# Kernel tuning notes

Hardware: AMD Instinct MI355X
Metric: run time of the kernel (lower is better)

Reference implementation:

```python
import jax, jax.numpy as jnp
import numpy as np

D = 1024
NH = 16
HD = D // NH
DFF = 4 * D
EPS = 1e-5


def setup_inputs() -> dict:
    key = jax.random.key(0)
    ks = jax.random.split(key, 12)
    s = lambda fan_in: 1.0 / np.sqrt(fan_in)
    return {
        "x": jax.random.normal(ks[0], (2, 2048, D), dtype=jnp.float32),
        # weights stored [in, out] (transpose of torch Linear layout)
        "w_qkv": jax.random.uniform(ks[1], (D, 3 * D), minval=-s(D), maxval=s(D)),
        "w_proj": jax.random.uniform(ks[2], (D, D), minval=-s(D), maxval=s(D)),
        "ln1_w": jnp.ones((D,), jnp.float32),
        "ln1_b": jnp.zeros((D,), jnp.float32),
        "ln2_w": jnp.ones((D,), jnp.float32),
        "ln2_b": jnp.zeros((D,), jnp.float32),
        "fc1_w": jax.random.uniform(ks[3], (D, DFF), minval=-s(D), maxval=s(D)),
        "fc1_b": jax.random.uniform(ks[4], (DFF,), minval=-s(D), maxval=s(D)),
        "fc2_w": jax.random.uniform(ks[5], (DFF, D), minval=-s(DFF), maxval=s(DFF)),
        "fc2_b": jax.random.uniform(ks[6], (D,), minval=-s(DFF), maxval=s(DFF)),
    }


def _layernorm(x, w, b):
    mu = jnp.mean(x, axis=-1, keepdims=True)
    var = jnp.mean(jnp.square(x - mu), axis=-1, keepdims=True)
    return (x - mu) * jax.lax.rsqrt(var + EPS) * w + b


def _attn(x, w_qkv, w_proj):
    B, T, C = x.shape
    qkv = x @ w_qkv  # [B,T,3C]
    q, k, v = jnp.split(qkv, 3, axis=-1)
    q = q.reshape(B, T, NH, HD).transpose(0, 2, 1, 3)  # [B,nh,T,hd]
    k = k.reshape(B, T, NH, HD).transpose(0, 2, 1, 3)
    v = v.reshape(B, T, NH, HD).transpose(0, 2, 1, 3)
    att = jnp.einsum("bhqd,bhkd->bhqk", q, k) / np.sqrt(HD)
    causal = jnp.tril(jnp.ones((T, T), bool))
    att = jnp.where(causal, att, -jnp.inf)
    att = jax.nn.softmax(att, axis=-1)
    out = jnp.einsum("bhqk,bhkd->bhqd", att, v)
    out = out.transpose(0, 2, 1, 3).reshape(B, T, C)
    return out @ w_proj


def reference(x, w_qkv, w_proj, ln1_w, ln1_b, ln2_w, ln2_b, fc1_w, fc1_b, fc2_w, fc2_b):
    x = x + _attn(_layernorm(x, ln1_w, ln1_b), w_qkv, w_proj)
    h = _layernorm(x, ln2_w, ln2_b)
    h = jax.nn.gelu(h @ fc1_w + fc1_b, approximate=False) @ fc2_w + fc2_b
    return x + h
```

## Files before the change

kernel.cpp:

```cpp
#include <hip/hip_runtime.h>


typedef short  bf16x8 __attribute__((ext_vector_type(8)));
typedef short  bf16x4 __attribute__((ext_vector_type(4)));
typedef float  fx4    __attribute__((ext_vector_type(4)));
typedef int    ix2    __attribute__((ext_vector_type(2)));

#define DEV static __device__ __forceinline__

DEV short f2bf(float f) {
    unsigned u = __builtin_bit_cast(unsigned, f);
    u += 0x7fffu + ((u >> 16) & 1u);
    return (short)(u >> 16);
}

#define AS1(p) ((__attribute__((address_space(1))) void*)(p))
#define AS3(p) ((__attribute__((address_space(3))) void*)(p))

__global__ __launch_bounds__(256) void ln_kernel(const float* __restrict__ x,
                                                 const float* __restrict__ w,
                                                 const float* __restrict__ b,
                                                 short* __restrict__ out)
{
    int row = blockIdx.x;
    int tid = threadIdx.x;
    const float4 v = *(const float4*)(x + (size_t)row * 1024 + tid * 4);
    float s = v.x + v.y + v.z + v.w;
    float q = v.x * v.x + v.y * v.y + v.z * v.z + v.w * v.w;
#pragma unroll
    for (int off = 32; off > 0; off >>= 1) {
        s += __shfl_down(s, off);
        q += __shfl_down(q, off);
    }
    __shared__ float ls[4], lq[4];
    if ((tid & 63) == 0) { ls[tid >> 6] = s; lq[tid >> 6] = q; }
    __syncthreads();
    float S  = ls[0] + ls[1] + ls[2] + ls[3];
    float Q  = lq[0] + lq[1] + lq[2] + lq[3];
    float mu  = S * (1.0f / 1024.0f);
    float var = Q * (1.0f / 1024.0f) - mu * mu;
    float inv = rsqrtf(var + 1e-5f);
    float4 wv = *(const float4*)(w + tid * 4);
    float4 bv = *(const float4*)(b + tid * 4);
    bf16x4 o;
    o[0] = f2bf((v.x - mu) * inv * wv.x + bv.x);
    o[1] = f2bf((v.y - mu) * inv * wv.y + bv.y);
    o[2] = f2bf((v.z - mu) * inv * wv.z + bv.z);
    o[3] = f2bf((v.w - mu) * inv * wv.w + bv.w);
    *(bf16x4*)(out + (size_t)row * 1024 + tid * 4) = o;
}

__global__ __launch_bounds__(256) void transpose_f32_bf16(const float* __restrict__ in,
                                                          short* __restrict__ out,
                                                          int R, int C)
{
    __shared__ float tile[64][65];
    int c0 = blockIdx.x * 64, r0 = blockIdx.y * 64;
    int t  = threadIdx.x;
    int tx = t & 15, ty = t >> 4;
#pragma unroll
    for (int i = 0; i < 4; ++i) {
        int row = i * 16 + ty;
        float4 v = *(const float4*)(in + (size_t)(r0 + row) * C + c0 + tx * 4);
        tile[row][tx * 4 + 0] = v.x;
        tile[row][tx * 4 + 1] = v.y;
        tile[row][tx * 4 + 2] = v.z;
        tile[row][tx * 4 + 3] = v.w;
    }
    __syncthreads();
    int seg = t & 7;
#pragma unroll
    for (int p = 0; p < 2; ++p) {
        int orow = p * 32 + (t >> 3);
        bf16x8 o;
#pragma unroll
        for (int u = 0; u < 8; ++u)
            o[u] = f2bf(tile[seg * 8 + u][orow]);
        *(bf16x8*)(out + (size_t)(c0 + orow) * R + r0 + seg * 8) = o;
    }
}

__global__ void vt_extract(const short* __restrict__ qkv, short* __restrict__ vt)
{
    __shared__ short tile[32][33];
    int t0 = blockIdx.x * 32, d0 = blockIdx.y * 32;
    int bh = blockIdx.z;
    int tx = threadIdx.x, ty = threadIdx.y;
    size_t inbase  = (size_t)(bh >> 4) * 2048 * 3072 + 2048 + (bh & 15) * 64;
    size_t outbase = (size_t)bh * 64 * 2048;
#pragma unroll
    for (int dy = 0; dy < 32; dy += 8)
        tile[ty + dy][tx] = qkv[inbase + (size_t)(t0 + ty + dy) * 3072 + d0 + tx];
    __syncthreads();
#pragma unroll
    for (int dy = 0; dy < 32; dy += 8)
        vt[outbase + (size_t)(d0 + ty + dy) * 2048 + t0 + tx] = tile[tx][ty + dy];
}

template <int BM, int BN, int BK, int SWZ, int PIPE, bool BIAS, bool GELU, bool RESID, bool OUT_BF16, bool PARTIAL>
__global__ __launch_bounds__(2 * BM) void gemm_bt(const short* __restrict__ A,
                                                  const short* __restrict__ Bt,
                                                  void* __restrict__ Cout,
                                                  void* __restrict__ Cout2,
                                                  const float* __restrict__ bias,
                                                  const float* __restrict__ resid,
                                                  int M, int N, int K)
{
    constexpr int NJ  = BN / 32;
    constexpr int NW  = BM / 32;
    constexpr int GR  = BK / 8;
    constexpr int RPC = 512 / BK;
    constexpr int NA  = (BM * BK) / 512;
    constexpr int NB  = (BN * BK) / 512;
    constexpr int LPS = (NA + NB) / NW;
    __shared__ short As[2][BM * BK];
    __shared__ short Bs[2][BN * BK];
    int tid  = threadIdx.x;
    int lane = tid & 63, wv = tid >> 6;
    int quad = lane >> 4, l15 = lane & 15;
    int bx = blockIdx.x, by = blockIdx.y;
    if constexpr (SWZ) {
        int nx   = gridDim.x;
        int nper = nx * gridDim.y;
        int flat = bx + nx * by;
        int cpx  = nper >> 3;
        int swz  = (flat & 7) * cpx + (flat >> 3);
        bx = swz % nx;
        by = swz / nx;
    }
    int m0 = by * BM, n0 = bx * BN;
    int SK   = gridDim.z;
    int kbeg = blockIdx.z * (K / SK);
    int NK   = (K / SK) / BK;
    int wr = (wv >> 1) * 64, wc = (wv & 1) * (BN / 2);
    fx4 acc[4][NJ] = {};
    int srow = lane / GR;
    int gl   = lane % GR;
    int fr   = (l15 >> 1) & (GR - 1);
    const short* Ab = A  + (size_t)m0 * K;
    const short* Bb = Bt + (size_t)n0 * K;

    auto stage = [&](int buf, int k0) {
#pragma unroll
        for (int c = wv; c < NA; c += NW) {
            int row  = c * RPC + srow;
            int scol = (gl ^ ((row >> 1) & (GR - 1))) * 8;
            __builtin_amdgcn_global_load_lds(AS1(Ab + (size_t)row * K + k0 + scol),
                                             AS3(&As[buf][c * 512]), 16, 0, 0);
        }
#pragma unroll
        for (int c = wv; c < NB; c += NW) {
            int row  = c * RPC + srow;
            int scol = (gl ^ ((row >> 1) & (GR - 1))) * 8;
            __builtin_amdgcn_global_load_lds(AS1(Bb + (size_t)row * K + k0 + scol),
                                             AS3(&Bs[buf][c * 512]), 16, 0, 0);
        }
    };

    auto compute_tile = [&](int cur) {
#pragma unroll
        for (int h = 0; h < BK / 32; ++h) {
            int rg = ((h * 4 + quad) ^ fr) * 8;
            bf16x8 af[4], bfr[NJ];
#pragma unroll
            for (int i = 0; i < 4; ++i)
                af[i] = *(const bf16x8*)&As[cur][(wr + i * 16 + l15) * BK + rg];
#pragma unroll
            for (int j = 0; j < NJ; ++j)
                bfr[j] = *(const bf16x8*)&Bs[cur][(wc + j * 16 + l15) * BK + rg];
#pragma unroll
            for (int i = 0; i < 4; ++i)
#pragma unroll
                for (int j = 0; j < NJ; ++j)
                    acc[i][j] = __builtin_amdgcn_mfma_f32_16x16x32_bf16(af[i], bfr[j], acc[i][j], 0, 0, 0);
        }
    };

    stage(0, kbeg);
    if constexpr (PIPE) {
        for (int kt = 0; kt < NK; ++kt) {
            int cur = kt & 1;
            if (kt + 1 < NK) {
                stage(cur ^ 1, kbeg + (kt + 1) * BK);
                if constexpr      (LPS == 3) asm volatile("s_waitcnt vmcnt(3)" ::: "memory");
                else if constexpr (LPS == 4) asm volatile("s_waitcnt vmcnt(4)" ::: "memory");
                else if constexpr (LPS == 8) asm volatile("s_waitcnt vmcnt(8)" ::: "memory");
                else                         asm volatile("s_waitcnt vmcnt(0)" ::: "memory");
            } else {
                asm volatile("s_waitcnt vmcnt(0)" ::: "memory");
            }
            asm volatile("s_barrier" ::: "memory");
            compute_tile(cur);
            asm volatile("s_barrier" ::: "memory");
        }
    } else {
        __syncthreads();
        for (int kt = 0; kt < NK; ++kt) {
            int cur = kt & 1;
            if (kt + 1 < NK) stage(cur ^ 1, kbeg + (kt + 1) * BK);
            compute_tile(cur);
            __syncthreads();
        }
    }

    if constexpr (PARTIAL) {
        float* P = blockIdx.z ? (float*)Cout2 : (float*)Cout;
#pragma unroll
        for (int i = 0; i < 4; ++i)
#pragma unroll
            for (int j = 0; j < NJ; ++j)
#pragma unroll
                for (int r = 0; r < 4; ++r) {
                    int row = m0 + wr + i * 16 + quad * 4 + r;
                    int col = n0 + wc + j * 16 + l15;
                    P[(size_t)row * N + col] = acc[i][j][r];
                }
    } else {
#pragma unroll
        for (int i = 0; i < 4; ++i)
#pragma unroll
            for (int j = 0; j < NJ; ++j)
#pragma unroll
                for (int r = 0; r < 4; ++r) {
                    int row = m0 + wr + i * 16 + quad * 4 + r;
                    int col = n0 + wc + j * 16 + l15;
                    float v = acc[i][j][r];
                    if constexpr (BIAS)  v += bias[col];
                    if constexpr (GELU) {
                        float e = exp2f(v * -2.4554674f);
                        v = v * __builtin_amdgcn_rcpf(1.0f + e);
                    }
                    if constexpr (RESID) v += resid[(size_t)row * N + col];
                    if constexpr (OUT_BF16) ((short*)Cout)[(size_t)row * N + col] = f2bf(v);
                    else                    ((float*)Cout)[(size_t)row * N + col] = v;
                }
    }
}

template <bool BIAS>
__global__ __launch_bounds__(256) void reduce2(const float* p0,
                                               const float* p1,
                                               const float* resid,
                                               const float* bias,
                                               float* out, int N)
{
    size_t idx = ((size_t)blockIdx.x * 256 + threadIdx.x) * 4;
    float4 a = *(const float4*)(p0 + idx);
    float4 b = *(const float4*)(p1 + idx);
    float4 r = *(const float4*)(resid + idx);
    float4 v;
    v.x = a.x + b.x + r.x; v.y = a.y + b.y + r.y;
    v.z = a.z + b.z + r.z; v.w = a.w + b.w + r.w;
    if constexpr (BIAS) {
        const float4 bv = *(const float4*)(bias + (idx & (N - 1)));
        v.x += bv.x; v.y += bv.y; v.z += bv.z; v.w += bv.w;
    }
    *(float4*)(out + idx) = v;
}

__global__ __launch_bounds__(256) void reduce2_ln(const float* __restrict__ p0,
                                                  const float* __restrict__ p1,
                                                  const float* __restrict__ resid,
                                                  const float* __restrict__ lw,
                                                  const float* __restrict__ lb,
                                                  float* __restrict__ out_f32,
                                                  short* __restrict__ out_bf16)
{
    int row = blockIdx.x, tid = threadIdx.x;
    size_t idx = (size_t)row * 1024 + tid * 4;
    float4 a = *(const float4*)(p0 + idx);
    float4 b = *(const float4*)(p1 + idx);
    float4 r = *(const float4*)(resid + idx);
    float4 v;
    v.x = a.x + b.x + r.x; v.y = a.y + b.y + r.y;
    v.z = a.z + b.z + r.z; v.w = a.w + b.w + r.w;
    *(float4*)(out_f32 + idx) = v;
    float s = v.x + v.y + v.z + v.w;
    float q = v.x * v.x + v.y * v.y + v.z * v.z + v.w * v.w;
#pragma unroll
    for (int off = 32; off > 0; off >>= 1) {
        s += __shfl_down(s, off);
        q += __shfl_down(q, off);
    }
    __shared__ float ls[4], lq[4];
    if ((tid & 63) == 0) { ls[tid >> 6] = s; lq[tid >> 6] = q; }
    __syncthreads();
    float S  = ls[0] + ls[1] + ls[2] + ls[3];
    float Q  = lq[0] + lq[1] + lq[2] + lq[3];
    float mu  = S * (1.0f / 1024.0f);
    float var = Q * (1.0f / 1024.0f) - mu * mu;
    float inv = rsqrtf(var + 1e-5f);
    float4 wv = *(const float4*)(lw + tid * 4);
    float4 bv = *(const float4*)(lb + tid * 4);
    bf16x4 o;
    o[0] = f2bf((v.x - mu) * inv * wv.x + bv.x);
    o[1] = f2bf((v.y - mu) * inv * wv.y + bv.y);
    o[2] = f2bf((v.z - mu) * inv * wv.z + bv.z);
    o[3] = f2bf((v.w - mu) * inv * wv.w + bv.w);
    *(bf16x4*)(out_bf16 + idx) = o;
}

__global__ __launch_bounds__(256) void attn_kernel(const short* __restrict__ qkv,
                                                   const short* __restrict__ vt,
                                                   short* __restrict__ out)
{
    __shared__ short Ks[2][64 * 64];
    __shared__ short Vs[2][64 * 64];
    const float CS = 0.125f * 1.44269504088896f;
    int tid  = threadIdx.x, lane = tid & 63, wv = tid >> 6;
    int quad = lane >> 4, l15 = lane & 15;
    int b = blockIdx.z, h = blockIdx.y, j = blockIdx.x;

    const short* kq = qkv + (size_t)b * 2048 * 3072 + 1024 + h * 64;
    const short* vb = vt  + (size_t)(b * 16 + h) * 64 * 2048;
    int srow = lane >> 3;
    int scol = ((lane & 7) ^ srow) * 8;
    int rg0  = (quad ^ (l15 & 7)) * 8;
    const bf16x4 vones = {(short)0x3F80, (short)0x3F80, (short)0x3F80, (short)0x3F80};

    for (int item = 0; item < 2; ++item) {
        int qt = item ? j : 31 - j;
        int q0 = qt * 64;
        int ktmax = qt;

        bf16x8 qf[2];
#pragma unroll
        for (int ks = 0; ks < 2; ++ks)
            qf[ks] = *(const bf16x8*)&qkv[(size_t)(b * 2048 + q0 + wv * 16 + l15) * 3072
                                           + h * 64 + ks * 32 + quad * 8];
        fx4 oacc[4] = {};
        fx4 lacc = {};

#pragma unroll
        for (int c = wv; c < 8; c += 4) {
            int row = c * 8 + srow;
            __builtin_amdgcn_global_load_lds(AS1(kq + (size_t)row * 3072 + scol),
                                             AS3(&Ks[0][c * 512]), 16, 0, 0);
            __builtin_amdgcn_global_load_lds(AS1(vb + (size_t)row * 2048 + scol),
                                             AS3(&Vs[0][c * 512]), 16, 0, 0);
        }
        __syncthreads();

        for (int kt = 0; kt <= ktmax; ++kt) {
            int cur = kt & 1;
            if (kt < ktmax) {
                int nb = cur ^ 1, tn = (kt + 1) * 64;
#pragma unroll
                for (int c = wv; c < 8; c += 4) {
                    int row = c * 8 + srow;
                    __builtin_amdgcn_global_load_lds(AS1(kq + (size_t)(tn + row) * 3072 + scol),
                                                     AS3(&Ks[nb][c * 512]), 16, 0, 0);
                    __builtin_amdgcn_global_load_lds(AS1(vb + (size_t)row * 2048 + tn + scol),
                                                     AS3(&Vs[nb][c * 512]), 16, 0, 0);
                }
            }

            fx4 s[4];
#pragma unroll
            for (int nt = 0; nt < 4; ++nt) {
                bf16x8 kf0 = *(const bf16x8*)&Ks[cur][(nt * 16 + l15) * 64 + rg0];
                bf16x8 kf1 = *(const bf16x8*)&Ks[cur][(nt * 16 + l15) * 64 + (rg0 ^ 32)];
                fx4 z = {0.f, 0.f, 0.f, 0.f};
                z = __builtin_amdgcn_mfma_f32_16x16x32_bf16(kf0, qf[0], z, 0, 0, 0);
                z = __builtin_amdgcn_mfma_f32_16x16x32_bf16(kf1, qf[1], z, 0, 0, 0);
                s[nt] = z;
            }
            if (kt == ktmax) {
                int delta = wv * 16 + l15;
#pragma unroll
                for (int nt = 0; nt < 4; ++nt)
#pragma unroll
                    for (int r = 0; r < 4; ++r)
                        if (nt * 16 + quad * 4 + r > delta) s[nt][r] = -1e30f;
            }

            bf16x4 pf[4];
#pragma unroll
            for (int nt = 0; nt < 4; ++nt) {
                float p0 = exp2f(s[nt][0] * CS);
                float p1 = exp2f(s[nt][1] * CS);
                float p2 = exp2f(s[nt][2] * CS);
                float p3 = exp2f(s[nt][3] * CS);
                unsigned a0 = __builtin_bit_cast(unsigned, p0) + 0x8000u;
                unsigned a1 = __builtin_bit_cast(unsigned, p1) + 0x8000u;
                unsigned a2 = __builtin_bit_cast(unsigned, p2) + 0x8000u;
                unsigned a3 = __builtin_bit_cast(unsigned, p3) + 0x8000u;
                ix2 pk;
                pk[0] = (int)__builtin_amdgcn_perm(a1, a0, 0x07060302u);
                pk[1] = (int)__builtin_amdgcn_perm(a3, a2, 0x07060302u);
                pf[nt] = __builtin_bit_cast(bf16x4, pk);
            }
#pragma unroll
            for (int nt = 0; nt < 4; ++nt)
                lacc = __builtin_amdgcn_mfma_f32_16x16x16bf16_1k(pf[nt], vones, lacc, 0, 0, 0);
#pragma unroll
            for (int dt = 0; dt < 4; ++dt) {
                int vrow  = dt * 16 + l15;
                int rbase = vrow * 64 + (quad & 1) * 4;
                int rk    = vrow & 7;
#pragma unroll
                for (int nt = 0; nt < 4; ++nt) {
                    int g = (nt * 2 + (quad >> 1)) ^ rk;
                    bf16x4 vf = *(const bf16x4*)&Vs[cur][rbase + g * 8];
                    oacc[dt] = __builtin_amdgcn_mfma_f32_16x16x16bf16_1k(pf[nt], vf, oacc[dt], 0, 0, 0);
                }
            }
            __syncthreads();
        }

        float linv[4];
#pragma unroll
        for (int r = 0; r < 4; ++r) linv[r] = 1.0f / lacc[r];
#pragma unroll
        for (int dt = 0; dt < 4; ++dt)
#pragma unroll
            for (int r = 0; r < 4; ++r) {
                int row = q0 + wv * 16 + quad * 4 + r;
                int col = h * 64 + dt * 16 + l15;
                out[((size_t)b * 2048 + row) * 1024 + col] = f2bf(oacc[dt][r] * linv[r]);
            }
    }
}

extern "C" void kernel_launch(void* const* d_in, const int* in_sizes, int n_in,
                              void* d_out, int out_size, void* d_ws, size_t ws_size,
                              hipStream_t stream)
{
    const float* x      = (const float*)d_in[0];
    const float* w_qkv  = (const float*)d_in[1];
    const float* w_proj = (const float*)d_in[2];
    const float* ln1_w  = (const float*)d_in[3];
    const float* ln1_b  = (const float*)d_in[4];
    const float* ln2_w  = (const float*)d_in[5];
    const float* ln2_b  = (const float*)d_in[6];
    const float* fc1_w  = (const float*)d_in[7];
    const float* fc1_b  = (const float*)d_in[8];
    const float* fc2_w  = (const float*)d_in[9];
    const float* fc2_b  = (const float*)d_in[10];
    float* out = (float*)d_out;
    char*  ws  = (char*)d_ws;

    size_t off = 0;
    auto alloc = [&](size_t bytes) { void* p = ws + off; off += (bytes + 255) & ~(size_t)255; return p; };
    short* tw_qkv  = (short*)alloc((size_t)3072 * 1024 * 2);
    short* tw_proj = (short*)alloc((size_t)1024 * 1024 * 2);
    short* tfc1    = (short*)alloc((size_t)4096 * 1024 * 2);
    short* tfc2    = (short*)alloc((size_t)1024 * 4096 * 2);
    short* xn      = (short*)alloc((size_t)4096 * 1024 * 2);
    short* qkvb    = (short*)alloc((size_t)4096 * 3072 * 2);
    short* vtb     = (short*)alloc((size_t)32 * 64 * 2048 * 2);
    short* attnb   = (short*)alloc((size_t)4096 * 1024 * 2);
    float* x1      = (float*)alloc((size_t)4096 * 1024 * 4);
    float* pk      = (float*)alloc((size_t)4096 * 1024 * 4);
    short* h1      = qkvb;

    transpose_f32_bf16<<<dim3(3072 / 64, 1024 / 64), 256, 0, stream>>>(w_qkv, tw_qkv, 1024, 3072);
    transpose_f32_bf16<<<dim3(1024 / 64, 1024 / 64), 256, 0, stream>>>(w_proj, tw_proj, 1024, 1024);
    transpose_f32_bf16<<<dim3(4096 / 64, 1024 / 64), 256, 0, stream>>>(fc1_w, tfc1, 1024, 4096);
    transpose_f32_bf16<<<dim3(1024 / 64, 4096 / 64), 256, 0, stream>>>(fc2_w, tfc2, 4096, 1024);

    ln_kernel<<<4096, 256, 0, stream>>>(x, ln1_w, ln1_b, xn);
    gemm_bt<256, 128, 32, 0, 1, false, false, false, true, false><<<dim3(24, 16, 1), 512, 0, stream>>>(
        xn, tw_qkv, qkvb, nullptr, nullptr, nullptr, 4096, 3072, 1024);
    vt_extract<<<dim3(2048 / 32, 64 / 32, 32), dim3(32, 8), 0, stream>>>(qkvb, vtb);
    attn_kernel<<<dim3(16, 16, 2), 256, 0, stream>>>(qkvb, vtb, attnb);
    gemm_bt<128, 64, 32, 0, 1, false, false, false, false, true><<<dim3(16, 32, 2), 256, 0, stream>>>(
        attnb, tw_proj, x1, pk, nullptr, nullptr, 4096, 1024, 1024);
    reduce2_ln<<<4096, 256, 0, stream>>>(x1, pk, x, ln2_w, ln2_b, x1, xn);
    gemm_bt<256, 128, 32, 0, 1, true, true, false, true, false><<<dim3(32, 16, 1), 512, 0, stream>>>(
        xn, tfc1, h1, nullptr, fc1_b, nullptr, 4096, 4096, 1024);
    gemm_bt<128, 128, 64, 1, 1, false, false, false, false, true><<<dim3(8, 32, 2), 256, 0, stream>>>(
        h1, tfc2, out, pk, nullptr, nullptr, 4096, 1024, 4096);
    reduce2<true><<<4096, 256, 0, stream>>>(out, pk, x1, fc2_b, out, 1024);
}
```

Baseline: 336.4 us.

## Process two 64-key tiles per pipeline stage in attention kernel

```diff
diff --git a/kernel.cpp b/kernel.cpp
--- a/kernel.cpp
+++ b/kernel.cpp
@@ -304,8 +304,8 @@
                                                    const short* __restrict__ vt,
                                                    short* __restrict__ out)
 {
-    __shared__ short Ks[2][64 * 64];
-    __shared__ short Vs[2][64 * 64];
+    __shared__ short Ks[2][2][64 * 64];
+    __shared__ short Vs[2][2][64 * 64];
     const float CS = 0.125f * 1.44269504088896f;
     int tid  = threadIdx.x, lane = tid & 63, wv = tid >> 6;
     int quad = lane >> 4, l15 = lane & 15;
@@ -321,7 +321,7 @@
     for (int item = 0; item < 2; ++item) {
         int qt = item ? j : 31 - j;
         int q0 = qt * 64;
-        int ktmax = qt;
+        int nkt = (qt >> 1) + 1;
 
         bf16x8 qf[2];
 #pragma unroll
@@ -332,77 +332,85 @@
         fx4 lacc = {};
 
 #pragma unroll
-        for (int c = wv; c < 8; c += 4) {
-            int row = c * 8 + srow;
-            __builtin_amdgcn_global_load_lds(AS1(kq + (size_t)row * 3072 + scol),
-                                             AS3(&Ks[0][c * 512]), 16, 0, 0);
-            __builtin_amdgcn_global_load_lds(AS1(vb + (size_t)row * 2048 + scol),
-                                             AS3(&Vs[0][c * 512]), 16, 0, 0);
-        }
+        for (int hh = 0; hh < 2; ++hh)
+            for (int c = wv; c < 8; c += 4) {
+                int row = c * 8 + srow;
+                __builtin_amdgcn_global_load_lds(AS1(kq + (size_t)(hh * 64 + row) * 3072 + scol),
+                                                 AS3(&Ks[0][hh][c * 512]), 16, 0, 0);
+                __builtin_amdgcn_global_load_lds(AS1(vb + (size_t)row * 2048 + hh * 64 + scol),
+                                                 AS3(&Vs[0][hh][c * 512]), 16, 0, 0);
+            }
         __syncthreads();
 
-        for (int kt = 0; kt <= ktmax; ++kt) {
+        for (int kt = 0; kt < nkt; ++kt) {
             int cur = kt & 1;
-            if (kt < ktmax) {
-                int nb = cur ^ 1, tn = (kt + 1) * 64;
-#pragma unroll
-                for (int c = wv; c < 8; c += 4) {
-                    int row = c * 8 + srow;
-                    __builtin_amdgcn_global_load_lds(AS1(kq + (size_t)(tn + row) * 3072 + scol),
-                                                     AS3(&Ks[nb][c * 512]), 16, 0, 0);
-                    __builtin_amdgcn_global_load_lds(AS1(vb + (size_t)row * 2048 + tn + scol),
-                                                     AS3(&Vs[nb][c * 512]), 16, 0, 0);
-                }
+            if (kt + 1 < nkt) {
+                int nb = cur ^ 1, tn = (kt + 1) * 128;
+#pragma unroll
+                for (int hh = 0; hh < 2; ++hh)
+                    for (int c = wv; c < 8; c += 4) {
+                        int row = c * 8 + srow;
+                        __builtin_amdgcn_global_load_lds(AS1(kq + (size_t)(tn + hh * 64 + row) * 3072 + scol),
+                                                         AS3(&Ks[nb][hh][c * 512]), 16, 0, 0);
+                        __builtin_amdgcn_global_load_lds(AS1(vb + (size_t)row * 2048 + tn + hh * 64 + scol),
+                                                         AS3(&Vs[nb][hh][c * 512]), 16, 0, 0);
+                    }
             }
 
-            fx4 s[4];
-#pragma unroll
-            for (int nt = 0; nt < 4; ++nt) {
-                bf16x8 kf0 = *(const bf16x8*)&Ks[cur][(nt * 16 + l15) * 64 + rg0];
-                bf16x8 kf1 = *(const bf16x8*)&Ks[cur][(nt * 16 + l15) * 64 + (rg0 ^ 32)];
-                fx4 z = {0.f, 0.f, 0.f, 0.f};
-                z = __builtin_amdgcn_mfma_f32_16x16x32_bf16(kf0, qf[0], z, 0, 0, 0);
-                z = __builtin_amdgcn_mfma_f32_16x16x32_bf16(kf1, qf[1], z, 0, 0, 0);
-                s[nt] = z;
-            }
-            if (kt == ktmax) {
-                int delta = wv * 16 + l15;
-#pragma unroll
-                for (int nt = 0; nt < 4; ++nt)
-#pragma unroll
-                    for (int r = 0; r < 4; ++r)
-                        if (nt * 16 + quad * 4 + r > delta) s[nt][r] = -1e30f;
-            }
-
-            bf16x4 pf[4];
-#pragma unroll
-            for (int nt = 0; nt < 4; ++nt) {
-                float p0 = exp2f(s[nt][0] * CS);
-                float p1 = exp2f(s[nt][1] * CS);
-                float p2 = exp2f(s[nt][2] * CS);
-                float p3 = exp2f(s[nt][3] * CS);
-                unsigned a0 = __builtin_bit_cast(unsigned, p0) + 0x8000u;
-                unsigned a1 = __builtin_bit_cast(unsigned, p1) + 0x8000u;
-                unsigned a2 = __builtin_bit_cast(unsigned, p2) + 0x8000u;
-                unsigned a3 = __builtin_bit_cast(unsigned, p3) + 0x8000u;
-                ix2 pk;
-                pk[0] = (int)__builtin_amdgcn_perm(a1, a0, 0x07060302u);
-                pk[1] = (int)__builtin_amdgcn_perm(a3, a2, 0x07060302u);
-                pf[nt] = __builtin_bit_cast(bf16x4, pk);
-            }
-#pragma unroll
-            for (int nt = 0; nt < 4; ++nt)
-                lacc = __builtin_amdgcn_mfma_f32_16x16x16bf16_1k(pf[nt], vones, lacc, 0, 0, 0);
-#pragma unroll
-            for (int dt = 0; dt < 4; ++dt) {
-                int vrow  = dt * 16 + l15;
-                int rbase = vrow * 64 + (quad & 1) * 4;
-                int rk    = vrow & 7;
-#pragma unroll
-                for (int nt = 0; nt < 4; ++nt) {
-                    int g = (nt * 2 + (quad >> 1)) ^ rk;
-                    bf16x4 vf = *(const bf16x4*)&Vs[cur][rbase + g * 8];
-                    oacc[dt] = __builtin_amdgcn_mfma_f32_16x16x16bf16_1k(pf[nt], vf, oacc[dt], 0, 0, 0);
+#pragma unroll
+            for (int hh = 0; hh < 2; ++hh) {
+                int kt2 = kt * 2 + hh;
+                if (kt2 <= qt) {
+                    fx4 s[4];
+#pragma unroll
+                    for (int nt = 0; nt < 4; ++nt) {
+                        bf16x8 kf0 = *(const bf16x8*)&Ks[cur][hh][(nt * 16 + l15) * 64 + rg0];
+                        bf16x8 kf1 = *(const bf16x8*)&Ks[cur][hh][(nt * 16 + l15) * 64 + (rg0 ^ 32)];
+                        fx4 z = {0.f, 0.f, 0.f, 0.f};
+                        z = __builtin_amdgcn_mfma_f32_16x16x32_bf16(kf0, qf[0], z, 0, 0, 0);
+                        z = __builtin_amdgcn_mfma_f32_16x16x32_bf16(kf1, qf[1], z, 0, 0, 0);
+                        s[nt] = z;
+                    }
+                    if (kt2 == qt) {
+                        int delta = wv * 16 + l15;
+#pragma unroll
+                        for (int nt = 0; nt < 4; ++nt)
+#pragma unroll
+                            for (int r = 0; r < 4; ++r)
+                                if (nt * 16 + quad * 4 + r > delta) s[nt][r] = -1e30f;
+                    }
+
+                    bf16x4 pf[4];
+#pragma unroll
+                    for (int nt = 0; nt < 4; ++nt) {
+                        float p0 = exp2f(s[nt][0] * CS);
+                        float p1 = exp2f(s[nt][1] * CS);
+                        float p2 = exp2f(s[nt][2] * CS);
+                        float p3 = exp2f(s[nt][3] * CS);
+                        unsigned a0 = __builtin_bit_cast(unsigned, p0) + 0x8000u;
+                        unsigned a1 = __builtin_bit_cast(unsigned, p1) + 0x8000u;
+                        unsigned a2 = __builtin_bit_cast(unsigned, p2) + 0x8000u;
+                        unsigned a3 = __builtin_bit_cast(unsigned, p3) + 0x8000u;
+                        ix2 pk;
+                        pk[0] = (int)__builtin_amdgcn_perm(a1, a0, 0x07060302u);
+                        pk[1] = (int)__builtin_amdgcn_perm(a3, a2, 0x07060302u);
+                        pf[nt] = __builtin_bit_cast(bf16x4, pk);
+                    }
+#pragma unroll
+                    for (int nt = 0; nt < 4; ++nt)
+                        lacc = __builtin_amdgcn_mfma_f32_16x16x16bf16_1k(pf[nt], vones, lacc, 0, 0, 0);
+#pragma unroll
+                    for (int dt = 0; dt < 4; ++dt) {
+                        int vrow  = dt * 16 + l15;
+                        int rbase = vrow * 64 + (quad & 1) * 4;
+                        int rk    = vrow & 7;
+#pragma unroll
+                        for (int nt = 0; nt < 4; ++nt) {
+                            int g = (nt * 2 + (quad >> 1)) ^ rk;
+                            bf16x4 vf = *(const bf16x4*)&Vs[cur][hh][rbase + g * 8];
+                            oacc[dt] = __builtin_amdgcn_mfma_f32_16x16x16bf16_1k(pf[nt], vf, oacc[dt], 0, 0, 0);
+                        }
+                    }
                 }
             }
             __syncthreads();
```

Result: slower. 350.2 us (+4.1%).

## Share K/V tile loads between paired causal query tiles in attention

Applied to the files above, without the earlier changes.

```diff
diff --git a/kernel.cpp b/kernel.cpp
--- a/kernel.cpp
+++ b/kernel.cpp
@@ -310,6 +310,10 @@
     int tid  = threadIdx.x, lane = tid & 63, wv = tid >> 6;
     int quad = lane >> 4, l15 = lane & 15;
     int b = blockIdx.z, h = blockIdx.y, j = blockIdx.x;
+    int jj = b ? (15 - j) : j;
+    int qt_hi = 31 - jj, qt_lo = jj;
+    int q0_hi = qt_hi * 64, q0_lo = qt_lo * 64;
+    int nkt = qt_hi + 1;
 
     const short* kq = qkv + (size_t)b * 2048 * 3072 + 1024 + h * 64;
     const short* vb = vt  + (size_t)(b * 16 + h) * 64 * 2048;
@@ -318,108 +322,113 @@
     int rg0  = (quad ^ (l15 & 7)) * 8;
     const bf16x4 vones = {(short)0x3F80, (short)0x3F80, (short)0x3F80, (short)0x3F80};
 
-    for (int item = 0; item < 2; ++item) {
-        int qt = item ? j : 31 - j;
-        int q0 = qt * 64;
-        int ktmax = qt;
-
-        bf16x8 qf[2];
-#pragma unroll
-        for (int ks = 0; ks < 2; ++ks)
-            qf[ks] = *(const bf16x8*)&qkv[(size_t)(b * 2048 + q0 + wv * 16 + l15) * 3072
-                                           + h * 64 + ks * 32 + quad * 8];
-        fx4 oacc[4] = {};
-        fx4 lacc = {};
-
-#pragma unroll
-        for (int c = wv; c < 8; c += 4) {
-            int row = c * 8 + srow;
-            __builtin_amdgcn_global_load_lds(AS1(kq + (size_t)row * 3072 + scol),
-                                             AS3(&Ks[0][c * 512]), 16, 0, 0);
-            __builtin_amdgcn_global_load_lds(AS1(vb + (size_t)row * 2048 + scol),
-                                             AS3(&Vs[0][c * 512]), 16, 0, 0);
-        }
+    bf16x8 qfh[2], qfl[2];
+#pragma unroll
+    for (int ks = 0; ks < 2; ++ks) {
+        qfh[ks] = *(const bf16x8*)&qkv[(size_t)(b * 2048 + q0_hi + wv * 16 + l15) * 3072
+                                        + h * 64 + ks * 32 + quad * 8];
+        qfl[ks] = *(const bf16x8*)&qkv[(size_t)(b * 2048 + q0_lo + wv * 16 + l15) * 3072
+                                        + h * 64 + ks * 32 + quad * 8];
+    }
+    fx4 oh[4] = {}, ol[4] = {};
+    fx4 lh = {}, ll = {};
+
+#pragma unroll
+    for (int c = wv; c < 8; c += 4) {
+        int row = c * 8 + srow;
+        __builtin_amdgcn_global_load_lds(AS1(kq + (size_t)row * 3072 + scol),
+                                         AS3(&Ks[0][c * 512]), 16, 0, 0);
+        __builtin_amdgcn_global_load_lds(AS1(vb + (size_t)row * 2048 + scol),
+                                         AS3(&Vs[0][c * 512]), 16, 0, 0);
+    }
+    __syncthreads();
+
+    auto body = [&](const bf16x8 (&qf)[2], fx4 (&oacc)[4], fx4& lacc,
+                    int qt, int kt, int cur) {
+        fx4 s[4];
+#pragma unroll
+        for (int nt = 0; nt < 4; ++nt) {
+            bf16x8 kf0 = *(const bf16x8*)&Ks[cur][(nt * 16 + l15) * 64 + rg0];
+            bf16x8 kf1 = *(const bf16x8*)&Ks[cur][(nt * 16 + l15) * 64 + (rg0 ^ 32)];
+            fx4 z = {0.f, 0.f, 0.f, 0.f};
+            z = __builtin_amdgcn_mfma_f32_16x16x32_bf16(kf0, qf[0], z, 0, 0, 0);
+            z = __builtin_amdgcn_mfma_f32_16x16x32_bf16(kf1, qf[1], z, 0, 0, 0);
+            s[nt] = z;
+        }
+        if (kt == qt) {
+            int delta = wv * 16 + l15;
+#pragma unroll
+            for (int nt = 0; nt < 4; ++nt)
+#pragma unroll
+                for (int r = 0; r < 4; ++r)
+                    if (nt * 16 + quad * 4 + r > delta) s[nt][r] = -1e30f;
+        }
+
+        bf16x4 pf[4];
+#pragma unroll
+        for (int nt = 0; nt < 4; ++nt) {
+            float p0 = exp2f(s[nt][0] * CS);
+            float p1 = exp2f(s[nt][1] * CS);
+            float p2 = exp2f(s[nt][2] * CS);
+            float p3 = exp2f(s[nt][3] * CS);
+            unsigned a0 = __builtin_bit_cast(unsigned, p0) + 0x8000u;
+            unsigned a1 = __builtin_bit_cast(unsigned, p1) + 0x8000u;
+            unsigned a2 = __builtin_bit_cast(unsigned, p2) + 0x8000u;
+            unsigned a3 = __builtin_bit_cast(unsigned, p3) + 0x8000u;
+            ix2 pk;
+            pk[0] = (int)__builtin_amdgcn_perm(a1, a0, 0x07060302u);
+            pk[1] = (int)__builtin_amdgcn_perm(a3, a2, 0x07060302u);
+            pf[nt] = __builtin_bit_cast(bf16x4, pk);
+        }
+#pragma unroll
+        for (int nt = 0; nt < 4; ++nt)
+            lacc = __builtin_amdgcn_mfma_f32_16x16x16bf16_1k(pf[nt], vones, lacc, 0, 0, 0);
+#pragma unroll
+        for (int dt = 0; dt < 4; ++dt) {
+            int vrow  = dt * 16 + l15;
+            int rbase = vrow * 64 + (quad & 1) * 4;
+            int rk    = vrow & 7;
+#pragma unroll
+            for (int nt = 0; nt < 4; ++nt) {
+                int g = (nt * 2 + (quad >> 1)) ^ rk;
+                bf16x4 vf = *(const bf16x4*)&Vs[cur][rbase + g * 8];
+                oacc[dt] = __builtin_amdgcn_mfma_f32_16x16x16bf16_1k(pf[nt], vf, oacc[dt], 0, 0, 0);
+            }
+        }
+    };
+
+    for (int kt = 0; kt < nkt; ++kt) {
+        int cur = kt & 1;
+        if (kt + 1 < nkt) {
+            int nb = cur ^ 1, tn = (kt + 1) * 64;
+#pragma unroll
+            for (int c = wv; c < 8; c += 4) {
+                int row = c * 8 + srow;
+                __builtin_amdgcn_global_load_lds(AS1(kq + (size_t)(tn + row) * 3072 + scol),
+                                                 AS3(&Ks[nb][c * 512]), 16, 0, 0);
+                __builtin_amdgcn_global_load_lds(AS1(vb + (size_t)row * 2048 + tn + scol),
+                                                 AS3(&Vs[nb][c * 512]), 16, 0, 0);
+            }
+        }
+
+        body(qfh, oh, lh, qt_hi, kt, cur);
+        if (kt <= qt_lo) body(qfl, ol, ll, qt_lo, kt, cur);
         __syncthreads();
-
-        for (int kt = 0; kt <= ktmax; ++kt) {
-            int cur = kt & 1;
-            if (kt < ktmax) {
-                int nb = cur ^ 1, tn = (kt + 1) * 64;
-#pragma unroll
-                for (int c = wv; c < 8; c += 4) {
-                    int row = c * 8 + srow;
-                    __builtin_amdgcn_global_load_lds(AS1(kq + (size_t)(tn + row) * 3072 + scol),
-                                                     AS3(&Ks[nb][c * 512]), 16, 0, 0);
-                    __builtin_amdgcn_global_load_lds(AS1(vb + (size_t)row * 2048 + tn + scol),
-                                                     AS3(&Vs[nb][c * 512]), 16, 0, 0);
-                }
-            }
-
-            fx4 s[4];
-#pragma unroll
-            for (int nt = 0; nt < 4; ++nt) {
-                bf16x8 kf0 = *(const bf16x8*)&Ks[cur][(nt * 16 + l15) * 64 + rg0];
-                bf16x8 kf1 = *(const bf16x8*)&Ks[cur][(nt * 16 + l15) * 64 + (rg0 ^ 32)];
-                fx4 z = {0.f, 0.f, 0.f, 0.f};
-                z = __builtin_amdgcn_mfma_f32_16x16x32_bf16(kf0, qf[0], z, 0, 0, 0);
-                z = __builtin_amdgcn_mfma_f32_16x16x32_bf16(kf1, qf[1], z, 0, 0, 0);
-                s[nt] = z;
-            }
-            if (kt == ktmax) {
-                int delta = wv * 16 + l15;
-#pragma unroll
-                for (int nt = 0; nt < 4; ++nt)
-#pragma unroll
-                    for (int r = 0; r < 4; ++r)
-                        if (nt * 16 + quad * 4 + r > delta) s[nt][r] = -1e30f;
-            }
-
-            bf16x4 pf[4];
-#pragma unroll
-            for (int nt = 0; nt < 4; ++nt) {
-                float p0 = exp2f(s[nt][0] * CS);
-                float p1 = exp2f(s[nt][1] * CS);
-                float p2 = exp2f(s[nt][2] * CS);
-                float p3 = exp2f(s[nt][3] * CS);
-                unsigned a0 = __builtin_bit_cast(unsigned, p0) + 0x8000u;
-                unsigned a1 = __builtin_bit_cast(unsigned, p1) + 0x8000u;
-                unsigned a2 = __builtin_bit_cast(unsigned, p2) + 0x8000u;
-                unsigned a3 = __builtin_bit_cast(unsigned, p3) + 0x8000u;
-                ix2 pk;
-                pk[0] = (int)__builtin_amdgcn_perm(a1, a0, 0x07060302u);
-                pk[1] = (int)__builtin_amdgcn_perm(a3, a2, 0x07060302u);
-                pf[nt] = __builtin_bit_cast(bf16x4, pk);
-            }
-#pragma unroll
-            for (int nt = 0; nt < 4; ++nt)
-                lacc = __builtin_amdgcn_mfma_f32_16x16x16bf16_1k(pf[nt], vones, lacc, 0, 0, 0);
-#pragma unroll
-            for (int dt = 0; dt < 4; ++dt) {
-                int vrow  = dt * 16 + l15;
-                int rbase = vrow * 64 + (quad & 1) * 4;
-                int rk    = vrow & 7;
-#pragma unroll
-                for (int nt = 0; nt < 4; ++nt) {
-                    int g = (nt * 2 + (quad >> 1)) ^ rk;
-                    bf16x4 vf = *(const bf16x4*)&Vs[cur][rbase + g * 8];
-                    oacc[dt] = __builtin_amdgcn_mfma_f32_16x16x16bf16_1k(pf[nt], vf, oacc[dt], 0, 0, 0);
-                }
-            }
-            __syncthreads();
-        }
-
-        float linv[4];
-#pragma unroll
-        for (int r = 0; r < 4; ++r) linv[r] = 1.0f / lacc[r];
-#pragma unroll
-        for (int dt = 0; dt < 4; ++dt)
-#pragma unroll
-            for (int r = 0; r < 4; ++r) {
-                int row = q0 + wv * 16 + quad * 4 + r;
-                int col = h * 64 + dt * 16 + l15;
-                out[((size_t)b * 2048 + row) * 1024 + col] = f2bf(oacc[dt][r] * linv[r]);
-            }
-    }
+    }
+
+    float lih[4], lil[4];
+#pragma unroll
+    for (int r = 0; r < 4; ++r) { lih[r] = 1.0f / lh[r]; lil[r] = 1.0f / ll[r]; }
+#pragma unroll
+    for (int dt = 0; dt < 4; ++dt)
+#pragma unroll
+        for (int r = 0; r < 4; ++r) {
+            int rowh = q0_hi + wv * 16 + quad * 4 + r;
+            int rowl = q0_lo + wv * 16 + quad * 4 + r;
+            int col  = h * 64 + dt * 16 + l15;
+            out[((size_t)b * 2048 + rowh) * 1024 + col] = f2bf(oh[dt][r] * lih[r]);
+            out[((size_t)b * 2048 + rowl) * 1024 + col] = f2bf(ol[dt][r] * lil[r]);
+        }
 }
 
 extern "C" void kernel_launch(void* const* d_in, const int* in_sizes, int n_in,
```

Measured after the change: 330.3 us. Within noise of the previous version (-1.8%).
